# Performance work log

Hardware: AMD Instinct MI355X
Metric: run time of the kernel (lower is better)

Reference implementation:

```python
import jax, jax.numpy as jnp
import numpy as np

BATCH, T, N_STATE, N_CTRL = 16, 512, 64, 32


def setup_inputs() -> dict:
    key = jax.random.key(0)
    ks = jax.random.split(key, 6)
    n, m = N_STATE, N_CTRL
    # SPD per-step cost: Q = M M^T/(n+m) + I  (guarantees Q_uu invertible)
    M = jax.random.normal(ks[0], (BATCH, T, n + m, n + m), jnp.float32)
    Q = jnp.einsum('btij,btkj->btik', M, M) / (n + m) + jnp.eye(n + m, dtype=jnp.float32)
    p = jax.random.normal(ks[1], (BATCH, T, n + m), jnp.float32)
    # near-stable dynamics so the T-step rollout stays bounded
    A = 0.9 * jnp.eye(n, dtype=jnp.float32) + 0.02 * jax.random.normal(ks[2], (BATCH, T, n, n), jnp.float32)
    B = 0.1 * jax.random.normal(ks[3], (BATCH, T, n, m), jnp.float32)
    c1 = 0.1 * jax.random.normal(ks[4], (BATCH, T, n), jnp.float32)
    x_init = jax.random.normal(ks[5], (BATCH, n), jnp.float32)
    return {'Q': Q, 'p': p, 'A': A, 'B': B, 'c1': c1, 'x_init': x_init}


def _lqr(Q, p, A, B, c1, x_init):
    n = A.shape[-1]
    F = jnp.concatenate([A, B], axis=-1)                      # [b,T,n,n+m]
    # time-major for scan
    Qs = jnp.moveaxis(Q, 1, 0)
    ps = jnp.moveaxis(p, 1, 0)
    Fs = jnp.moveaxis(F, 1, 0)
    cs = jnp.moveaxis(c1, 1, 0)
    bsz = x_init.shape[0]
    V0 = jnp.zeros((bsz, n, n), Q.dtype)
    v0 = jnp.zeros((bsz, n), Q.dtype)

    def bstep(carry, inp):
        V, v = carry
        Qt, pt, Ft, ct = inp
        FtV = jnp.einsum('bij,bik->bjk', Ft, V)               # F^T V : [b,n+m,n]
        Qh = Qt + FtV @ Ft                                     # Q_t + F^T V F
        qh = pt + jnp.einsum('bij,bi->bj', Ft,
                             jnp.einsum('bij,bj->bi', V, ct) + v)
        Quu, Qux = Qh[:, n:, n:], Qh[:, n:, :n]
        Qxx, Qxu = Qh[:, :n, :n], Qh[:, :n, n:]
        qx, qu = qh[:, :n], qh[:, n:]
        L = jnp.linalg.cholesky(Quu)
        rhs = jnp.concatenate([Qux, qu[..., None]], axis=-1)   # solve K and k together
        sol = -jax.scipy.linalg.cho_solve((L, True), rhs)
        K, k = sol[..., :n], sol[..., n]
        QuuK = Quu @ K
        Vn = Qxx + Qxu @ K + jnp.einsum('bji,bjk->bik', K, Qux + QuuK)
        Vn = 0.5 * (Vn + jnp.swapaxes(Vn, -1, -2))             # keep symmetric
        vn = qx + jnp.einsum('bij,bj->bi', Qxu, k) \
             + jnp.einsum('bji,bj->bi', K, qu + jnp.einsum('bij,bj->bi', Quu, k))
        return (Vn, vn), (K, k)

    _, (Ks, ks) = jax.lax.scan(bstep, (V0, v0), (Qs, ps, Fs, cs), reverse=True)

    def fstep(x, inp):
        Kt, kt, At, Bt, ct = inp
        u = jnp.einsum('bij,bj->bi', Kt, x) + kt
        xn = jnp.einsum('bij,bj->bi', At, x) + jnp.einsum('bij,bj->bi', Bt, u) + ct
        return xn, (x, u)

    _, (xs, us) = jax.lax.scan(fstep, x_init,
                               (Ks, ks, jnp.moveaxis(A, 1, 0), jnp.moveaxis(B, 1, 0), cs))
    tau = jnp.concatenate([xs, us], axis=-1)                   # [T,b,n+m]
    return jnp.moveaxis(tau, 0, 1)                             # [b,T,n+m]


def reference(Q, p, A, B, c1, x_init):
    return _lqr(Q, p, A, B, c1, x_init)
```

## Files before the change

kernel.cpp:

```cpp
#include <hip/hip_runtime.h>
#include <math.h>

#define TT 512
#define NB 16

#define QH_B   0
#define LI_B   38400
#define T1_B   43008
#define VBH_B  52368
#define VBL_B  61584
#define FTH_B  70800
#define FTL_B  84624
#define WTH_B  98448
#define WTL_B  112272
#define VR_B   98448
#define XUH_B  126096
#define XUL_B  131216
#define KTH_B  136336
#define KTL_B  141456
#define QHF_B  146576
#define VV_B   146960
#define CV_B   147216
#define KV_B   147472
#define SMB    147600

#define AB0 0
#define AB1 6400
#define KF0 12800
#define KF1 14976
#define XB0 17152
#define XB1 17216
#define UBO 17280
#define AXO 17312

#define WSK_STRIDE 2080

typedef __attribute__((ext_vector_type(8))) short s8v;
typedef __attribute__((ext_vector_type(4))) float f4v;

__device__ __forceinline__ float lanebc(float x, int lane) {
    return __int_as_float(__builtin_amdgcn_readlane(__float_as_int(x), lane));
}
__device__ __forceinline__ float dot4(float4 a, float4 b) {
    return a.x * b.x + a.y * b.y + a.z * b.z + a.w * b.w;
}
__device__ __forceinline__ unsigned short f2bf(float x) {
    unsigned int u = __float_as_uint(x);
    u += 0x7FFFu + ((u >> 16) & 1u);
    return (unsigned short)(u >> 16);
}
__device__ __forceinline__ float bf2f(unsigned short h) {
    return __uint_as_float(((unsigned int)h) << 16);
}
__device__ __forceinline__ void tileMN(int T, int& mt, int& nt) {
    mt = (T >= 15) ? 5 : (T >= 10) ? 4 : (T >= 6) ? 3 : (T >= 3) ? 2 : (T >= 1) ? 1 : 0;
    nt = T - mt * (mt + 1) / 2;
}
#define MFMA(a,b,c) __builtin_amdgcn_mfma_f32_16x16x32_bf16((a),(b),(c),0,0,0)

__launch_bounds__(512, 2)
__global__ void lqr_kernel(const float* __restrict__ Q, const float* __restrict__ P,
                           const float* __restrict__ A, const float* __restrict__ B,
                           const float* __restrict__ c1, const float* __restrict__ xinit,
                           float* __restrict__ out, float* __restrict__ ws)
{
    __shared__ __align__(16) unsigned char smb[SMB];
    float*          QHf = (float*)(smb + QH_B);
    float*          LIf = (float*)(smb + LI_B);
    float*          T1f = (float*)(smb + T1_B);
    unsigned short* VBH = (unsigned short*)(smb + VBH_B);
    unsigned short* VBL = (unsigned short*)(smb + VBL_B);
    unsigned short* FTH = (unsigned short*)(smb + FTH_B);
    unsigned short* FTL = (unsigned short*)(smb + FTL_B);
    unsigned short* WTH = (unsigned short*)(smb + WTH_B);
    unsigned short* WTL = (unsigned short*)(smb + WTL_B);
    float*          VRW = (float*)(smb + VR_B);
    unsigned short* XUH = (unsigned short*)(smb + XUH_B);
    unsigned short* XUL = (unsigned short*)(smb + XUL_B);
    unsigned short* KTH = (unsigned short*)(smb + KTH_B);
    unsigned short* KTL = (unsigned short*)(smb + KTL_B);
    float*          QHF = (float*)(smb + QHF_B);
    float*          VVf = (float*)(smb + VV_B);
    float*          CVf = (float*)(smb + CV_B);
    float*          KVf = (float*)(smb + KV_B);

    const int tid = threadIdx.x;
    const int b   = blockIdx.x;
    const int wv  = tid >> 6;
    const int ln  = tid & 63;
    const int l15 = ln & 15;
    const int lq  = ln >> 4;
    float* wsK = ws;

    const int qcnt = (wv < 5) ? 3 : 2;
    const int qr = ln >> 2, qc4 = ln & 3;

    float4 qreg[3];
    {
        const float* Qg = Q + ((size_t)b * TT + (TT - 1)) * 9216;
        for (int tt = 0; tt < qcnt; ++tt) {
            int T = wv + 8 * tt, mt, nt; tileMN(T, mt, nt);
            qreg[tt] = *(const float4*)&Qg[(16 * mt + qr) * 96 + 16 * nt + 4 * qc4];
        }
    }

    if (tid < 384) {
        const size_t bt = (size_t)b * TT + (TT - 1);
        const int kk = tid & 63, cq = tid >> 6;
#pragma unroll
        for (int q = 0; q < 4; ++q) {
            const float* src = (cq < 4) ? (A + (bt * 64 + kk) * 64 + 16 * cq + 4 * q)
                                        : (B + (bt * 64 + kk) * 32 + 16 * (cq - 4) + 4 * q);
            float4 v = *(const float4*)src;
#pragma unroll
            for (int e = 0; e < 4; ++e) {
                int col = 16 * cq + 4 * q + e;
                float x = (e == 0) ? v.x : (e == 1) ? v.y : (e == 2) ? v.z : v.w;
                unsigned short h = f2bf(x);
                FTH[col * 72 + kk] = h;
                FTL[col * 72 + kk] = f2bf(x - bf2f(h));
            }
        }
    } else {
        float* vb = (float*)VBH;
        for (int i = tid - 384; i < 4608; i += 128) vb[i] = 0.0f;
        if (tid >= 448) VVf[tid - 448] = 0.0f;
    }
    __syncthreads();

    for (int t = TT - 1; t >= 0; --t) {
        const size_t bt  = (size_t)b * TT + t;
        const size_t btp = (size_t)b * TT + ((t > 0) ? (t - 1) : 0);

        for (int tt = 0; tt < qcnt; ++tt) {
            int T = wv + 8 * tt, mt, nt; tileMN(T, mt, nt);
            *(float4*)&QHf[(16 * mt + qr) * 100 + 16 * nt + 4 * qc4] = qreg[tt];
        }
        {
            const float* Qg = Q + btp * 9216;
            for (int tt = 0; tt < qcnt; ++tt) {
                int T = wv + 8 * tt, mt, nt; tileMN(T, mt, nt);
                qreg[tt] = *(const float4*)&Qg[(16 * mt + qr) * 96 + 16 * nt + 4 * qc4];
            }
        }
        float4 fp4[4];
        if (wv >= 1 && wv <= 6) {
            const int tau = tid - 64, kk = tau & 63, cq = tau >> 6;
#pragma unroll
            for (int q = 0; q < 4; ++q) {
                const float* src = (cq < 4) ? (A + (btp * 64 + kk) * 64 + 16 * cq + 4 * q)
                                            : (B + (btp * 64 + kk) * 32 + 16 * (cq - 4) + 4 * q);
                fp4[q] = *(const float4*)src;
            }
        }
        if (wv == 7 && ln < 16)
            *(float4*)&CVf[4 * ln] = *(const float4*)&c1[bt * 64 + 4 * ln];
        float pv = 0.0f;
        if (ln < 48 && (ln & 3) == 0) pv = P[bt * 96 + 12 * wv + (ln >> 2)];

        {
#pragma unroll
            for (int tt = 0; tt < 3; ++tt) {
                int T = wv * 3 + tt, mt = T >> 2, nt = T & 3;
                const unsigned short* ah = FTH + (16 * mt + l15) * 72 + 8 * lq;
                const unsigned short* al = FTL + (16 * mt + l15) * 72 + 8 * lq;
                const unsigned short* bh = VBH + (16 * nt + l15) * 72 + 8 * lq;
                const unsigned short* bl = VBL + (16 * nt + l15) * 72 + 8 * lq;
                f4v d = {0.0f, 0.0f, 0.0f, 0.0f};
#pragma unroll
                for (int kc = 0; kc < 2; ++kc) {
                    s8v Ah = *(const s8v*)(ah + 32 * kc);
                    s8v Al = *(const s8v*)(al + 32 * kc);
                    s8v Bh = *(const s8v*)(bh + 32 * kc);
                    s8v Bl = *(const s8v*)(bl + 32 * kc);
                    d = MFMA(Ah, Bh, d);
                    d = MFMA(Ah, Bl, d);
                    d = MFMA(Al, Bh, d);
                }
                int orow = 16 * mt + 4 * lq, ocol = 16 * nt + l15;
#pragma unroll
                for (int rr = 0; rr < 4; ++rr) {
                    float x = d[rr];
                    unsigned short h = f2bf(x);
                    WTH[(orow + rr) * 72 + ocol] = h;
                    WTL[(orow + rr) * 72 + ocol] = f2bf(x - bf2f(h));
                }
            }
            if (ln < 48) {
                int row = 12 * wv + (ln >> 2), kq = ln & 3;
                float acc = 0.0f;
                const unsigned short* fh = FTH + row * 72 + 16 * kq;
                const unsigned short* fl = FTL + row * 72 + 16 * kq;
                const float* vvp = VVf + 16 * kq;
#pragma unroll
                for (int k = 0; k < 16; ++k)
                    acc += (bf2f(fh[k]) + bf2f(fl[k])) * vvp[k];
                acc += __shfl_xor(acc, 1);
                acc += __shfl_xor(acc, 2);
                if ((ln & 3) == 0) QHF[row] = acc + pv;
            }
        }
        __syncthreads();

        {
            for (int tt = 0; tt < qcnt; ++tt) {
                int T = wv + 8 * tt, mt, nt; tileMN(T, mt, nt);
                int orow = 16 * mt + 4 * lq, ocol = 16 * nt + l15;
                const unsigned short* ah = FTH + (16 * mt + l15) * 72 + 8 * lq;
                const unsigned short* al = FTL + (16 * mt + l15) * 72 + 8 * lq;
                const unsigned short* bh = WTH + (16 * nt + l15) * 72 + 8 * lq;
                const unsigned short* bl = WTL + (16 * nt + l15) * 72 + 8 * lq;
                f4v d;
#pragma unroll
                for (int rr = 0; rr < 4; ++rr)
                    d[rr] = QHf[(orow + rr) * 100 + ocol];
#pragma unroll
                for (int kc = 0; kc < 2; ++kc) {
                    s8v Ah = *(const s8v*)(ah + 32 * kc);
                    s8v Al = *(const s8v*)(al + 32 * kc);
                    s8v Bh = *(const s8v*)(bh + 32 * kc);
                    s8v Bl = *(const s8v*)(bl + 32 * kc);
                    d = MFMA(Ah, Bh, d);
                    d = MFMA(Ah, Bl, d);
                    d = MFMA(Al, Bh, d);
                }
#pragma unroll
                for (int rr = 0; rr < 4; ++rr)
                    QHf[(orow + rr) * 100 + ocol] = d[rr];
                if (mt > nt) {
#pragma unroll
                    for (int rr = 0; rr < 4; ++rr)
                        QHf[ocol * 100 + orow + rr] = d[rr];
                }
                if (mt >= 4 && nt < 4) {
#pragma unroll
                    for (int rr = 0; rr < 4; ++rr) {
                        float x = d[rr];
                        unsigned short h = f2bf(x);
                        XUH[ocol * 40 + (orow + rr - 64)] = h;
                        XUL[ocol * 40 + (orow + rr - 64)] = f2bf(x - bf2f(h));
                    }
                }
            }
        }
        __syncthreads();

        if (wv == 0) {
            const int i = ln & 31;
            float a[32], rinv[32];
#pragma unroll
            for (int j4 = 0; j4 < 8; ++j4) {
                float4 v = *(const float4*)&QHf[(64 + i) * 100 + 64 + 4 * j4];
                a[4 * j4] = v.x; a[4 * j4 + 1] = v.y; a[4 * j4 + 2] = v.z; a[4 * j4 + 3] = v.w;
            }
#pragma unroll
            for (int j = 0; j < 32; ++j) {
                float dj = lanebc(a[j], j);
                float rj = rsqrtf(dj);
                rinv[j] = rj;
                a[j] *= rj;
#pragma unroll
                for (int k = j + 1; k < 32; ++k)
                    a[k] -= a[j] * lanebc(a[j], k);
            }
            float y[32];
#pragma unroll
            for (int r = 0; r < 32; ++r) {
                float acc0 = (r == i) ? 1.0f : 0.0f, acc1 = 0.0f;
#pragma unroll
                for (int j = 0; j < r; ++j) {
                    float lrj = lanebc(a[j], r);
                    if (j & 1) acc1 -= lrj * y[j]; else acc0 -= lrj * y[j];
                }
                y[r] = (acc0 + acc1) * rinv[r];
            }
            if (ln < 32) {
#pragma unroll
                for (int r = 0; r < 32; ++r) LIf[r * 36 + ln] = y[r];
            }
        } else if (wv == 7) {
#pragma unroll
            for (int pass = 0; pass < 2; ++pass) {
                int j = pass ? (64 + (ln & 31)) : ln;
                if (pass && ln >= 32) break;
                float acc = QHF[j];
                const unsigned short* wh = WTH + j * 72;
                const unsigned short* wl = WTL + j * 72;
#pragma unroll 4
                for (int i = 0; i < 64; ++i)
                    acc += (bf2f(wh[i]) + bf2f(wl[i])) * CVf[i];
                QHf[j * 100 + 96] = acc;
            }
        } else {
            const int tau = tid - 64, kk = tau & 63, cq = tau >> 6;
#pragma unroll
            for (int q = 0; q < 4; ++q) {
                float4 v = fp4[q];
#pragma unroll
                for (int e = 0; e < 4; ++e) {
                    int col = 16 * cq + 4 * q + e;
                    float x = (e == 0) ? v.x : (e == 1) ? v.y : (e == 2) ? v.z : v.w;
                    unsigned short h = f2bf(x);
                    FTH[col * 72 + kk] = h;
                    FTL[col * 72 + kk] = f2bf(x - bf2f(h));
                }
            }
        }
        __syncthreads();

        {
            const int c = tid & 63, rq = tid >> 6;
            f4v acc = {0.0f, 0.0f, 0.0f, 0.0f};
#pragma unroll
            for (int j4 = 0; j4 < 8; ++j4) {
                float4 qv = *(const float4*)&QHf[c * 100 + 64 + 4 * j4];
#pragma unroll
                for (int rr = 0; rr < 4; ++rr) {
                    float4 li = *(const float4*)&LIf[(4 * rq + rr) * 36 + 4 * j4];
                    acc[rr] += dot4(li, qv);
                }
            }
            *(f4v*)&T1f[c * 36 + 4 * rq] = acc;
            if (tid < 32) {
                float aq = 0.0f;
#pragma unroll 4
                for (int j = 0; j < 32; ++j)
                    aq += LIf[tid * 36 + j] * QHf[(64 + j) * 100 + 96];
                T1f[64 * 36 + tid] = aq;
            }
        }
        __syncthreads();

        {
            const int c = tid & 63, jq = tid >> 6;
            f4v acc = {0.0f, 0.0f, 0.0f, 0.0f};
#pragma unroll
            for (int i4 = 0; i4 < 8; ++i4) {
                float4 tv = *(const float4*)&T1f[c * 36 + 4 * i4];
#pragma unroll
                for (int ii = 0; ii < 4; ++ii) {
                    float4 li = *(const float4*)&LIf[(4 * i4 + ii) * 36 + 4 * jq];
                    float tvi = (ii == 0) ? tv.x : (ii == 1) ? tv.y : (ii == 2) ? tv.z : tv.w;
                    acc[0] += tvi * li.x; acc[1] += tvi * li.y;
                    acc[2] += tvi * li.z; acc[3] += tvi * li.w;
                }
            }
            float* wrow = wsK + bt * WSK_STRIDE;
#pragma unroll
            for (int jj = 0; jj < 4; ++jj) {
                float kval = -acc[jj];
                unsigned short h = f2bf(kval);
                KTH[c * 40 + 4 * jq + jj] = h;
                KTL[c * 40 + 4 * jq + jj] = f2bf(kval - bf2f(h));
                wrow[(4 * jq + jj) * 65 + c] = kval;
            }
            if (tid < 32) {
                float aq = 0.0f;
#pragma unroll 4
                for (int i = 0; i < 32; ++i)
                    aq += LIf[i * 36 + tid] * T1f[64 * 36 + i];
                KVf[tid] = -aq;
                wsK[bt * WSK_STRIDE + tid * 65 + 64] = -aq;
            }
        }
        __syncthreads();

        {
#pragma unroll
            for (int tt = 0; tt < 2; ++tt) {
                int T = 2 * wv + tt, mt = T >> 2, nt = T & 3;
                int orow = 16 * mt + 4 * lq, ocol = 16 * nt + l15;
                f4v d;
#pragma unroll
                for (int rr = 0; rr < 4; ++rr)
                    d[rr] = QHf[(orow + rr) * 100 + ocol];
                s8v Ah = *(const s8v*)(XUH + (16 * mt + l15) * 40 + 8 * lq);
                s8v Al = *(const s8v*)(XUL + (16 * mt + l15) * 40 + 8 * lq);
                s8v Bh = *(const s8v*)(KTH + (16 * nt + l15) * 40 + 8 * lq);
                s8v Bl = *(const s8v*)(KTL + (16 * nt + l15) * 40 + 8 * lq);
                d = MFMA(Ah, Bh, d);
                d = MFMA(Ah, Bl, d);
                d = MFMA(Al, Bh, d);
#pragma unroll
                for (int rr = 0; rr < 4; ++rr)
                    VRW[(orow + rr) * 72 + ocol] = d[rr];
            }
        }
        __syncthreads();

        if (tid < 256) {
            const int rg = tid >> 4, cgv = tid & 15;
            float4 m0[4], m1[4];
#pragma unroll
            for (int rr = 0; rr < 4; ++rr) {
                m0[rr] = *(const float4*)&VRW[(4 * rg + rr) * 72 + 4 * cgv];
                m1[rr] = *(const float4*)&VRW[(4 * cgv + rr) * 72 + 4 * rg];
            }
#pragma unroll
            for (int rr = 0; rr < 4; ++rr) {
                float s[4];
                s[0] = 0.5f * (m0[rr].x + ((float*)&m1[0])[rr]);
                s[1] = 0.5f * (m0[rr].y + ((float*)&m1[1])[rr]);
                s[2] = 0.5f * (m0[rr].z + ((float*)&m1[2])[rr]);
                s[3] = 0.5f * (m0[rr].w + ((float*)&m1[3])[rr]);
                unsigned short h[4], lo[4];
#pragma unroll
                for (int cc = 0; cc < 4; ++cc) {
                    h[cc]  = f2bf(s[cc]);
                    lo[cc] = f2bf(s[cc] - bf2f(h[cc]));
                }
                ushort4 hv = make_ushort4(h[0], h[1], h[2], h[3]);
                ushort4 lv = make_ushort4(lo[0], lo[1], lo[2], lo[3]);
                *(ushort4*)&VBH[(4 * rg + rr) * 72 + 4 * cgv] = hv;
                *(ushort4*)&VBL[(4 * rg + rr) * 72 + 4 * cgv] = lv;
            }
        } else if (tid < 320) {
            const int r = tid & 63;
            float acc = QHf[r * 100 + 96];
#pragma unroll
            for (int j4 = 0; j4 < 8; ++j4) {
                float4 qv = *(const float4*)&QHf[r * 100 + 64 + 4 * j4];
                float4 kv = *(const float4*)&KVf[4 * j4];
                acc += dot4(qv, kv);
            }
            VVf[r] = acc;
        }
        __syncthreads();
    }

    float* sm = (float*)smb;
    {
        const size_t bt0 = (size_t)b * TT;
#pragma unroll
        for (int it = 0; it < 3; ++it) {
            int q = tid + 512 * it, row = q / 24, g = q % 24;
            const float* src = (g < 16) ? (A + (bt0 * 64 + row) * 64 + 4 * g)
                                        : (B + (bt0 * 64 + row) * 32 + 4 * (g - 16));
            *(float4*)&sm[AB0 + row * 100 + 4 * g] = *(const float4*)src;
        }
#pragma unroll
        for (int i = 0; i < 5; ++i) {
            int idx = tid + 512 * i;
            if (idx < 2080) {
                int j = idx / 65, c = idx - 65 * j;
                sm[KF0 + j * 68 + c] = wsK[bt0 * WSK_STRIDE + idx];
            }
        }
        if (tid < 64) sm[XB0 + tid] = xinit[b * 64 + tid];
    }
    __syncthreads();

    for (int t = 0; t < TT; ++t) {
        const size_t bt  = (size_t)b * TT + t;
        const size_t btn = (size_t)b * TT + ((t < TT - 1) ? (t + 1) : t);
        const int cur = t & 1;
        const int abC = cur ? AB1 : AB0, abN = cur ? AB0 : AB1;
        const int kfC = cur ? KF1 : KF0, kfN = cur ? KF0 : KF1;
        const int xbC = cur ? XB1 : XB0, xbN = cur ? XB0 : XB1;

        float4 abpre[6];
        float kpre[9];
        float cpre = 0.0f;
        if (tid >= 256) {
            const int t2 = tid - 256;
#pragma unroll
            for (int it = 0; it < 6; ++it) {
                int q = t2 + 256 * it, row = q / 24, g = q % 24;
                const float* src = (g < 16) ? (A + (btn * 64 + row) * 64 + 4 * g)
                                            : (B + (btn * 64 + row) * 32 + 4 * (g - 16));
                abpre[it] = *(const float4*)src;
            }
#pragma unroll
            for (int i = 0; i < 9; ++i) {
                int idx = t2 + 256 * i;
                kpre[i] = (idx < 2080) ? wsK[btn * WSK_STRIDE + idx] : 0.0f;
            }
            cpre = c1[bt * 64 + ((tid - 256) >> 2)];
        }

        if (tid < 256) {
            const int j = tid >> 3, q = tid & 7;
            float4 k0 = *(const float4*)&sm[kfC + j * 68 + 8 * q];
            float4 k1 = *(const float4*)&sm[kfC + j * 68 + 8 * q + 4];
            float4 x0 = *(const float4*)&sm[xbC + 8 * q];
            float4 x1 = *(const float4*)&sm[xbC + 8 * q + 4];
            float pa = dot4(k0, x0) + dot4(k1, x1);
            pa += __shfl_xor(pa, 1);
            pa += __shfl_xor(pa, 2);
            pa += __shfl_xor(pa, 4);
            if (q == 0) {
                float u = pa + sm[kfC + j * 68 + 64];
                sm[UBO + j] = u;
                out[bt * 96 + 64 + j] = u;
            }
        } else {
            const int r = (tid - 256) >> 2, q = tid & 3;
            float pa = 0.0f;
#pragma unroll
            for (int e4 = 0; e4 < 4; ++e4) {
                float4 av = *(const float4*)&sm[abC + r * 100 + 16 * q + 4 * e4];
                float4 xv = *(const float4*)&sm[xbC + 16 * q + 4 * e4];
                pa += dot4(av, xv);
            }
            pa += __shfl_xor(pa, 1);
            pa += __shfl_xor(pa, 2);
            if (q == 0) sm[AXO + r] = pa + cpre;
            if (q == 1) out[bt * 96 + r] = sm[xbC + r];
        }
        __syncthreads();

        if (tid < 256) {
            const int r = tid >> 2, q = tid & 3;
            float4 b0 = *(const float4*)&sm[abC + r * 100 + 64 + 8 * q];
            float4 b1 = *(const float4*)&sm[abC + r * 100 + 64 + 8 * q + 4];
            float4 u0 = *(const float4*)&sm[UBO + 8 * q];
            float4 u1 = *(const float4*)&sm[UBO + 8 * q + 4];
            float pa = dot4(b0, u0) + dot4(b1, u1);
            pa += __shfl_xor(pa, 1);
            pa += __shfl_xor(pa, 2);
            if (q == 0) sm[xbN + r] = sm[AXO + r] + pa;
        } else {
            const int t2 = tid - 256;
#pragma unroll
            for (int it = 0; it < 6; ++it) {
                int q = t2 + 256 * it, row = q / 24, g = q % 24;
                *(float4*)&sm[abN + row * 100 + 4 * g] = abpre[it];
            }
#pragma unroll
            for (int i = 0; i < 9; ++i) {
                int idx = t2 + 256 * i;
                if (idx < 2080) {
                    int j = idx / 65, c = idx - 65 * j;
                    sm[kfN + j * 68 + c] = kpre[i];
                }
            }
        }
        __syncthreads();
    }
}

extern "C" void kernel_launch(void* const* d_in, const int* in_sizes, int n_in,
                              void* d_out, int out_size, void* d_ws, size_t ws_size,
                              hipStream_t stream) {
    (void)in_sizes; (void)n_in; (void)out_size;
    const float* Q  = (const float*)d_in[0];
    const float* p  = (const float*)d_in[1];
    const float* A  = (const float*)d_in[2];
    const float* B  = (const float*)d_in[3];
    const float* c1 = (const float*)d_in[4];
    const float* xi = (const float*)d_in[5];
    if (ws_size < (size_t)NB * TT * WSK_STRIDE * sizeof(float)) return;
    lqr_kernel<<<NB, 512, 0, stream>>>(Q, p, A, B, c1, xi, (float*)d_out, (float*)d_ws);
}
```

Measured before the change: 9.074 ms.

## Double block size to 1024 threads and redistribute per-step work across 16 waves

Launches the single-block-per-batch LQR kernel with 1024 threads instead of 512 and reassigns every phase of the backward and forward recursions (Q tile loads, F^T V MFMA tiles, vector products, Cholesky-based gain products, V update tiles) across 16 waves. The aim is to shorten the per-timestep serial critical path, since only 16 blocks run and most of the GPU is idle. More threads per block means more barrier cost and less register budget per thread, and many phases now leave some waves idle.

```diff
diff --git a/kernel.cpp b/kernel.cpp
--- a/kernel.cpp
+++ b/kernel.cpp
@@ -58,7 +58,7 @@
 }
 #define MFMA(a,b,c) __builtin_amdgcn_mfma_f32_16x16x32_bf16((a),(b),(c),0,0,0)
 
-__launch_bounds__(512, 2)
+__launch_bounds__(1024, 4)
 __global__ void lqr_kernel(const float* __restrict__ Q, const float* __restrict__ P,
                            const float* __restrict__ A, const float* __restrict__ B,
                            const float* __restrict__ c1, const float* __restrict__ xinit,
@@ -92,29 +92,31 @@
     const int lq  = ln >> 4;
     float* wsK = ws;
 
-    const int qcnt = (wv < 5) ? 3 : 2;
+    const int qcnt = (wv < 5) ? 2 : 1;
     const int qr = ln >> 2, qc4 = ln & 3;
 
-    float4 qreg[3];
+    float4 qreg[2];
     {
         const float* Qg = Q + ((size_t)b * TT + (TT - 1)) * 9216;
-        for (int tt = 0; tt < qcnt; ++tt) {
-            int T = wv + 8 * tt, mt, nt; tileMN(T, mt, nt);
+#pragma unroll
+        for (int tt = 0; tt < 2; ++tt) if (tt < qcnt) {
+            int T = wv + 16 * tt, mt, nt; tileMN(T, mt, nt);
             qreg[tt] = *(const float4*)&Qg[(16 * mt + qr) * 96 + 16 * nt + 4 * qc4];
         }
     }
 
-    if (tid < 384) {
+    if (tid < 768) {
         const size_t bt = (size_t)b * TT + (TT - 1);
         const int kk = tid & 63, cq = tid >> 6;
 #pragma unroll
-        for (int q = 0; q < 4; ++q) {
-            const float* src = (cq < 4) ? (A + (bt * 64 + kk) * 64 + 16 * cq + 4 * q)
-                                        : (B + (bt * 64 + kk) * 32 + 16 * (cq - 4) + 4 * q);
+        for (int q = 0; q < 2; ++q) {
+            int col0 = 8 * cq + 4 * q;
+            const float* src = (col0 < 64) ? (A + (bt * 64 + kk) * 64 + col0)
+                                           : (B + (bt * 64 + kk) * 32 + col0 - 64);
             float4 v = *(const float4*)src;
 #pragma unroll
             for (int e = 0; e < 4; ++e) {
-                int col = 16 * cq + 4 * q + e;
+                int col = col0 + e;
                 float x = (e == 0) ? v.x : (e == 1) ? v.y : (e == 2) ? v.z : v.w;
                 unsigned short h = f2bf(x);
                 FTH[col * 72 + kk] = h;
@@ -123,8 +125,8 @@
         }
     } else {
         float* vb = (float*)VBH;
-        for (int i = tid - 384; i < 4608; i += 128) vb[i] = 0.0f;
-        if (tid >= 448) VVf[tid - 448] = 0.0f;
+        for (int i = tid - 768; i < 4608; i += 256) vb[i] = 0.0f;
+        if (tid >= 768 && tid < 832) VVf[tid - 768] = 0.0f;
     }
     __syncthreads();
 
@@ -132,36 +134,42 @@
         const size_t bt  = (size_t)b * TT + t;
         const size_t btp = (size_t)b * TT + ((t > 0) ? (t - 1) : 0);
 
-        for (int tt = 0; tt < qcnt; ++tt) {
-            int T = wv + 8 * tt, mt, nt; tileMN(T, mt, nt);
+#pragma unroll
+        for (int tt = 0; tt < 2; ++tt) if (tt < qcnt) {
+            int T = wv + 16 * tt, mt, nt; tileMN(T, mt, nt);
             *(float4*)&QHf[(16 * mt + qr) * 100 + 16 * nt + 4 * qc4] = qreg[tt];
         }
         {
             const float* Qg = Q + btp * 9216;
-            for (int tt = 0; tt < qcnt; ++tt) {
-                int T = wv + 8 * tt, mt, nt; tileMN(T, mt, nt);
+#pragma unroll
+            for (int tt = 0; tt < 2; ++tt) if (tt < qcnt) {
+                int T = wv + 16 * tt, mt, nt; tileMN(T, mt, nt);
                 qreg[tt] = *(const float4*)&Qg[(16 * mt + qr) * 96 + 16 * nt + 4 * qc4];
             }
         }
-        float4 fp4[4];
-        if (wv >= 1 && wv <= 6) {
+        float4 fp4[2];
+        if (wv >= 1 && wv <= 12) {
             const int tau = tid - 64, kk = tau & 63, cq = tau >> 6;
 #pragma unroll
-            for (int q = 0; q < 4; ++q) {
-                const float* src = (cq < 4) ? (A + (btp * 64 + kk) * 64 + 16 * cq + 4 * q)
-                                            : (B + (btp * 64 + kk) * 32 + 16 * (cq - 4) + 4 * q);
+            for (int q = 0; q < 2; ++q) {
+                int col0 = 8 * cq + 4 * q;
+                const float* src = (col0 < 64) ? (A + (btp * 64 + kk) * 64 + col0)
+                                               : (B + (btp * 64 + kk) * 32 + col0 - 64);
                 fp4[q] = *(const float4*)src;
             }
         }
-        if (wv == 7 && ln < 16)
+        if (wv == 13 && ln < 16)
             *(float4*)&CVf[4 * ln] = *(const float4*)&c1[bt * 64 + 4 * ln];
         float pv = 0.0f;
-        if (ln < 48 && (ln & 3) == 0) pv = P[bt * 96 + 12 * wv + (ln >> 2)];
+        if (wv < 12 && (ln & 7) == 0) pv = P[bt * 96 + 8 * wv + (ln >> 3)];
 
         {
-#pragma unroll
-            for (int tt = 0; tt < 3; ++tt) {
-                int T = wv * 3 + tt, mt = T >> 2, nt = T & 3;
+            int t1l[2]; int nT1;
+            if (wv < 8) { t1l[0] = 2 * wv; t1l[1] = 2 * wv + 1; nT1 = 2; }
+            else        { t1l[0] = 8 + wv; t1l[1] = 0;          nT1 = 1; }
+#pragma unroll
+            for (int tt = 0; tt < 2; ++tt) if (tt < nT1) {
+                int T = t1l[tt], mt = T >> 2, nt = T & 3;
                 const unsigned short* ah = FTH + (16 * mt + l15) * 72 + 8 * lq;
                 const unsigned short* al = FTL + (16 * mt + l15) * 72 + 8 * lq;
                 const unsigned short* bh = VBH + (16 * nt + l15) * 72 + 8 * lq;
@@ -186,25 +194,27 @@
                     WTL[(orow + rr) * 72 + ocol] = f2bf(x - bf2f(h));
                 }
             }
-            if (ln < 48) {
-                int row = 12 * wv + (ln >> 2), kq = ln & 3;
+            if (wv < 12) {
+                int row = 8 * wv + (ln >> 3), kq = ln & 7;
                 float acc = 0.0f;
-                const unsigned short* fh = FTH + row * 72 + 16 * kq;
-                const unsigned short* fl = FTL + row * 72 + 16 * kq;
-                const float* vvp = VVf + 16 * kq;
-#pragma unroll
-                for (int k = 0; k < 16; ++k)
+                const unsigned short* fh = FTH + row * 72 + 8 * kq;
+                const unsigned short* fl = FTL + row * 72 + 8 * kq;
+                const float* vvp = VVf + 8 * kq;
+#pragma unroll
+                for (int k = 0; k < 8; ++k)
                     acc += (bf2f(fh[k]) + bf2f(fl[k])) * vvp[k];
                 acc += __shfl_xor(acc, 1);
                 acc += __shfl_xor(acc, 2);
-                if ((ln & 3) == 0) QHF[row] = acc + pv;
+                acc += __shfl_xor(acc, 4);
+                if ((ln & 7) == 0) QHF[row] = acc + pv;
             }
         }
         __syncthreads();
 
         {
-            for (int tt = 0; tt < qcnt; ++tt) {
-                int T = wv + 8 * tt, mt, nt; tileMN(T, mt, nt);
+#pragma unroll
+            for (int tt = 0; tt < 2; ++tt) if (tt < qcnt) {
+                int T = wv + 16 * tt, mt, nt; tileMN(T, mt, nt);
                 int orow = 16 * mt + 4 * lq, ocol = 16 * nt + l15;
                 const unsigned short* ah = FTH + (16 * mt + l15) * 72 + 8 * lq;
                 const unsigned short* al = FTL + (16 * mt + l15) * 72 + 8 * lq;
@@ -278,11 +288,9 @@
 #pragma unroll
                 for (int r = 0; r < 32; ++r) LIf[r * 36 + ln] = y[r];
             }
-        } else if (wv == 7) {
-#pragma unroll
-            for (int pass = 0; pass < 2; ++pass) {
-                int j = pass ? (64 + (ln & 31)) : ln;
-                if (pass && ln >= 32) break;
+        } else if (wv >= 14) {
+            int j = (wv == 14) ? ln : (64 + (ln & 31));
+            if (wv == 14 || ln < 32) {
                 float acc = QHF[j];
                 const unsigned short* wh = WTH + j * 72;
                 const unsigned short* wl = WTL + j * 72;
@@ -291,14 +299,15 @@
                     acc += (bf2f(wh[i]) + bf2f(wl[i])) * CVf[i];
                 QHf[j * 100 + 96] = acc;
             }
-        } else {
+        } else if (wv <= 12) {
             const int tau = tid - 64, kk = tau & 63, cq = tau >> 6;
 #pragma unroll
-            for (int q = 0; q < 4; ++q) {
+            for (int q = 0; q < 2; ++q) {
                 float4 v = fp4[q];
+                int col0 = 8 * cq + 4 * q;
 #pragma unroll
                 for (int e = 0; e < 4; ++e) {
-                    int col = 16 * cq + 4 * q + e;
+                    int col = col0 + e;
                     float x = (e == 0) ? v.x : (e == 1) ? v.y : (e == 2) ? v.z : v.w;
                     unsigned short h = f2bf(x);
                     FTH[col * 72 + kk] = h;
@@ -309,18 +318,17 @@
         __syncthreads();
 
         {
-            const int c = tid & 63, rq = tid >> 6;
-            f4v acc = {0.0f, 0.0f, 0.0f, 0.0f};
+            const int c = tid & 63, g = tid >> 6;
+            float a0 = 0.0f, a1 = 0.0f;
 #pragma unroll
             for (int j4 = 0; j4 < 8; ++j4) {
                 float4 qv = *(const float4*)&QHf[c * 100 + 64 + 4 * j4];
-#pragma unroll
-                for (int rr = 0; rr < 4; ++rr) {
-                    float4 li = *(const float4*)&LIf[(4 * rq + rr) * 36 + 4 * j4];
-                    acc[rr] += dot4(li, qv);
-                }
-            }
-            *(f4v*)&T1f[c * 36 + 4 * rq] = acc;
+                float4 l0 = *(const float4*)&LIf[(2 * g) * 36 + 4 * j4];
+                float4 l1 = *(const float4*)&LIf[(2 * g + 1) * 36 + 4 * j4];
+                a0 += dot4(l0, qv);
+                a1 += dot4(l1, qv);
+            }
+            *(float2*)&T1f[c * 36 + 2 * g] = make_float2(a0, a1);
             if (tid < 32) {
                 float aq = 0.0f;
 #pragma unroll 4
@@ -332,28 +340,26 @@
         __syncthreads();
 
         {
-            const int c = tid & 63, jq = tid >> 6;
-            f4v acc = {0.0f, 0.0f, 0.0f, 0.0f};
+            const int c = tid & 63, g = tid >> 6;
+            float a0 = 0.0f, a1 = 0.0f;
 #pragma unroll
             for (int i4 = 0; i4 < 8; ++i4) {
                 float4 tv = *(const float4*)&T1f[c * 36 + 4 * i4];
 #pragma unroll
                 for (int ii = 0; ii < 4; ++ii) {
-                    float4 li = *(const float4*)&LIf[(4 * i4 + ii) * 36 + 4 * jq];
+                    float2 li = *(const float2*)&LIf[(4 * i4 + ii) * 36 + 2 * g];
                     float tvi = (ii == 0) ? tv.x : (ii == 1) ? tv.y : (ii == 2) ? tv.z : tv.w;
-                    acc[0] += tvi * li.x; acc[1] += tvi * li.y;
-                    acc[2] += tvi * li.z; acc[3] += tvi * li.w;
-                }
-            }
+                    a0 += tvi * li.x;
+                    a1 += tvi * li.y;
+                }
+            }
+            float k0 = -a0, k1 = -a1;
+            unsigned short h0 = f2bf(k0), h1 = f2bf(k1);
+            *(ushort2*)&KTH[c * 40 + 2 * g] = make_ushort2(h0, h1);
+            *(ushort2*)&KTL[c * 40 + 2 * g] = make_ushort2(f2bf(k0 - bf2f(h0)), f2bf(k1 - bf2f(h1)));
             float* wrow = wsK + bt * WSK_STRIDE;
-#pragma unroll
-            for (int jj = 0; jj < 4; ++jj) {
-                float kval = -acc[jj];
-                unsigned short h = f2bf(kval);
-                KTH[c * 40 + 4 * jq + jj] = h;
-                KTL[c * 40 + 4 * jq + jj] = f2bf(kval - bf2f(h));
-                wrow[(4 * jq + jj) * 65 + c] = kval;
-            }
+            wrow[(2 * g) * 65 + c]     = k0;
+            wrow[(2 * g + 1) * 65 + c] = k1;
             if (tid < 32) {
                 float aq = 0.0f;
 #pragma unroll 4
@@ -366,25 +372,22 @@
         __syncthreads();
 
         {
-#pragma unroll
-            for (int tt = 0; tt < 2; ++tt) {
-                int T = 2 * wv + tt, mt = T >> 2, nt = T & 3;
-                int orow = 16 * mt + 4 * lq, ocol = 16 * nt + l15;
-                f4v d;
-#pragma unroll
-                for (int rr = 0; rr < 4; ++rr)
-                    d[rr] = QHf[(orow + rr) * 100 + ocol];
-                s8v Ah = *(const s8v*)(XUH + (16 * mt + l15) * 40 + 8 * lq);
-                s8v Al = *(const s8v*)(XUL + (16 * mt + l15) * 40 + 8 * lq);
-                s8v Bh = *(const s8v*)(KTH + (16 * nt + l15) * 40 + 8 * lq);
-                s8v Bl = *(const s8v*)(KTL + (16 * nt + l15) * 40 + 8 * lq);
-                d = MFMA(Ah, Bh, d);
-                d = MFMA(Ah, Bl, d);
-                d = MFMA(Al, Bh, d);
-#pragma unroll
-                for (int rr = 0; rr < 4; ++rr)
-                    VRW[(orow + rr) * 72 + ocol] = d[rr];
-            }
+            int mt = wv >> 2, nt = wv & 3;
+            int orow = 16 * mt + 4 * lq, ocol = 16 * nt + l15;
+            f4v d;
+#pragma unroll
+            for (int rr = 0; rr < 4; ++rr)
+                d[rr] = QHf[(orow + rr) * 100 + ocol];
+            s8v Ah = *(const s8v*)(XUH + (16 * mt + l15) * 40 + 8 * lq);
+            s8v Al = *(const s8v*)(XUL + (16 * mt + l15) * 40 + 8 * lq);
+            s8v Bh = *(const s8v*)(KTH + (16 * nt + l15) * 40 + 8 * lq);
+            s8v Bl = *(const s8v*)(KTL + (16 * nt + l15) * 40 + 8 * lq);
+            d = MFMA(Ah, Bh, d);
+            d = MFMA(Ah, Bl, d);
+            d = MFMA(Al, Bh, d);
+#pragma unroll
+            for (int rr = 0; rr < 4; ++rr)
+                VRW[(orow + rr) * 72 + ocol] = d[rr];
         }
         __syncthreads();
 
@@ -432,15 +435,18 @@
     {
         const size_t bt0 = (size_t)b * TT;
 #pragma unroll
-        for (int it = 0; it < 3; ++it) {
-            int q = tid + 512 * it, row = q / 24, g = q % 24;
-            const float* src = (g < 16) ? (A + (bt0 * 64 + row) * 64 + 4 * g)
-                                        : (B + (bt0 * 64 + row) * 32 + 4 * (g - 16));
-            *(float4*)&sm[AB0 + row * 100 + 4 * g] = *(const float4*)src;
-        }
-#pragma unroll
-        for (int i = 0; i < 5; ++i) {
-            int idx = tid + 512 * i;
+        for (int it = 0; it < 2; ++it) {
+            int q = tid + 1024 * it;
+            if (q < 1536) {
+                int row = q / 24, g = q % 24;
+                const float* src = (g < 16) ? (A + (bt0 * 64 + row) * 64 + 4 * g)
+                                            : (B + (bt0 * 64 + row) * 32 + 4 * (g - 16));
+                *(float4*)&sm[AB0 + row * 100 + 4 * g] = *(const float4*)src;
+            }
+        }
+#pragma unroll
+        for (int i = 0; i < 3; ++i) {
+            int idx = tid + 1024 * i;
             if (idx < 2080) {
                 int j = idx / 65, c = idx - 65 * j;
                 sm[KF0 + j * 68 + c] = wsK[bt0 * WSK_STRIDE + idx];
@@ -461,8 +467,8 @@
         float4 abpre[6];
         float kpre[9];
         float cpre = 0.0f;
-        if (tid >= 256) {
-            const int t2 = tid - 256;
+        if (tid >= 512 && tid < 768) {
+            const int t2 = tid - 512;
 #pragma unroll
             for (int it = 0; it < 6; ++it) {
                 int q = t2 + 256 * it, row = q / 24, g = q % 24;
@@ -475,8 +481,9 @@
                 int idx = t2 + 256 * i;
                 kpre[i] = (idx < 2080) ? wsK[btn * WSK_STRIDE + idx] : 0.0f;
             }
+        }
+        if (tid >= 256 && tid < 512)
             cpre = c1[bt * 64 + ((tid - 256) >> 2)];
-        }
 
         if (tid < 256) {
             const int j = tid >> 3, q = tid & 7;
@@ -493,7 +500,7 @@
                 sm[UBO + j] = u;
                 out[bt * 96 + 64 + j] = u;
             }
-        } else {
+        } else if (tid < 512) {
             const int r = (tid - 256) >> 2, q = tid & 3;
             float pa = 0.0f;
 #pragma unroll
@@ -519,8 +526,8 @@
             pa += __shfl_xor(pa, 1);
             pa += __shfl_xor(pa, 2);
             if (q == 0) sm[xbN + r] = sm[AXO + r] + pa;
-        } else {
-            const int t2 = tid - 256;
+        } else if (tid >= 512 && tid < 768) {
+            const int t2 = tid - 512;
 #pragma unroll
             for (int it = 0; it < 6; ++it) {
                 int q = t2 + 256 * it, row = q / 24, g = q % 24;
@@ -550,5 +557,5 @@
     const float* c1 = (const float*)d_in[4];
     const float* xi = (const float*)d_in[5];
     if (ws_size < (size_t)NB * TT * WSK_STRIDE * sizeof(float)) return;
-    lqr_kernel<<<NB, 512, 0, stream>>>(Q, p, A, B, c1, xi, (float*)d_out, (float*)d_ws);
-}
+    lqr_kernel<<<NB, 1024, 0, stream>>>(Q, p, A, B, c1, xi, (float*)d_out, (float*)d_ws);
+}
```

After: 11.63 ms. +28.1%, slower.

## Restructure backward step schedule to cut barriers and rebalance wave work

Applied to the files above, without the earlier changes.

Qh tile products are redistributed so waves overlap them with the Cholesky wave, F-conversion is moved into the K-solve stage, and the two-stage K computation is merged into one stage using a transposed inverse-L copy. The separate symmetrization pass for V is dropped: V is written straight to bf16 hi/lo from the MFMA output, and the value-vector update uses a shuffle reduction. This removes two block barriers per time step and reshapes the shared-memory layout. Skipping explicit symmetrization means V relies on the algebraic symmetry of the result, which may slightly change numerics.

```diff
diff --git a/kernel.cpp b/kernel.cpp
--- a/kernel.cpp
+++ b/kernel.cpp
@@ -6,23 +6,23 @@
 
 #define QH_B   0
 #define LI_B   38400
-#define T1_B   43008
-#define VBH_B  52368
-#define VBL_B  61584
-#define FTH_B  70800
-#define FTL_B  84624
-#define WTH_B  98448
-#define WTL_B  112272
-#define VR_B   98448
-#define XUH_B  126096
-#define XUL_B  131216
-#define KTH_B  136336
-#define KTL_B  141456
-#define QHF_B  146576
-#define VV_B   146960
-#define CV_B   147216
-#define KV_B   147472
-#define SMB    147600
+#define LIT_B  43008
+#define KV_B   47616
+#define VBH_B  47744
+#define VBL_B  56960
+#define FTH_B  66176
+#define FTL_B  80000
+#define WTH_B  93824
+#define WTL_B  107648
+#define T1S_B  93824
+#define XUH_B  121472
+#define XUL_B  126592
+#define KTH_B  131712
+#define KTL_B  136832
+#define QHF_B  141952
+#define VV_B   142336
+#define CV_B   142592
+#define SMB    142848
 
 #define AB0 0
 #define AB1 6400
@@ -67,14 +67,14 @@
     __shared__ __align__(16) unsigned char smb[SMB];
     float*          QHf = (float*)(smb + QH_B);
     float*          LIf = (float*)(smb + LI_B);
-    float*          T1f = (float*)(smb + T1_B);
+    float*          LIT = (float*)(smb + LIT_B);
+    float*          T1S = (float*)(smb + T1S_B);
     unsigned short* VBH = (unsigned short*)(smb + VBH_B);
     unsigned short* VBL = (unsigned short*)(smb + VBL_B);
     unsigned short* FTH = (unsigned short*)(smb + FTH_B);
     unsigned short* FTL = (unsigned short*)(smb + FTL_B);
     unsigned short* WTH = (unsigned short*)(smb + WTH_B);
     unsigned short* WTL = (unsigned short*)(smb + WTL_B);
-    float*          VRW = (float*)(smb + VR_B);
     unsigned short* XUH = (unsigned short*)(smb + XUH_B);
     unsigned short* XUL = (unsigned short*)(smb + XUL_B);
     unsigned short* KTH = (unsigned short*)(smb + KTH_B);
@@ -98,7 +98,8 @@
     float4 qreg[3];
     {
         const float* Qg = Q + ((size_t)b * TT + (TT - 1)) * 9216;
-        for (int tt = 0; tt < qcnt; ++tt) {
+#pragma unroll
+        for (int tt = 0; tt < 3; ++tt) if (tt < qcnt) {
             int T = wv + 8 * tt, mt, nt; tileMN(T, mt, nt);
             qreg[tt] = *(const float4*)&Qg[(16 * mt + qr) * 96 + 16 * nt + 4 * qc4];
         }
@@ -132,20 +133,22 @@
         const size_t bt  = (size_t)b * TT + t;
         const size_t btp = (size_t)b * TT + ((t > 0) ? (t - 1) : 0);
 
-        for (int tt = 0; tt < qcnt; ++tt) {
+#pragma unroll
+        for (int tt = 0; tt < 3; ++tt) if (tt < qcnt) {
             int T = wv + 8 * tt, mt, nt; tileMN(T, mt, nt);
             *(float4*)&QHf[(16 * mt + qr) * 100 + 16 * nt + 4 * qc4] = qreg[tt];
         }
         {
             const float* Qg = Q + btp * 9216;
-            for (int tt = 0; tt < qcnt; ++tt) {
+#pragma unroll
+            for (int tt = 0; tt < 3; ++tt) if (tt < qcnt) {
                 int T = wv + 8 * tt, mt, nt; tileMN(T, mt, nt);
                 qreg[tt] = *(const float4*)&Qg[(16 * mt + qr) * 96 + 16 * nt + 4 * qc4];
             }
         }
         float4 fp4[4];
-        if (wv >= 1 && wv <= 6) {
-            const int tau = tid - 64, kk = tau & 63, cq = tau >> 6;
+        if (tid >= 128) {
+            const int tau = tid - 128, kk = tau & 63, cq = tau >> 6;
 #pragma unroll
             for (int q = 0; q < 4; ++q) {
                 const float* src = (cq < 4) ? (A + (btp * 64 + kk) * 64 + 16 * cq + 4 * q)
@@ -157,6 +160,46 @@
             *(float4*)&CVf[4 * ln] = *(const float4*)&c1[bt * 64 + 4 * ln];
         float pv = 0.0f;
         if (ln < 48 && (ln & 3) == 0) pv = P[bt * 96 + 12 * wv + (ln >> 2)];
+
+        auto qhTile = [&](int T) {
+            int mt, nt; tileMN(T, mt, nt);
+            int orow = 16 * mt + 4 * lq, ocol = 16 * nt + l15;
+            const unsigned short* ah = FTH + (16 * mt + l15) * 72 + 8 * lq;
+            const unsigned short* al = FTL + (16 * mt + l15) * 72 + 8 * lq;
+            const unsigned short* bh = WTH + (16 * nt + l15) * 72 + 8 * lq;
+            const unsigned short* bl = WTL + (16 * nt + l15) * 72 + 8 * lq;
+            f4v d;
+#pragma unroll
+            for (int rr = 0; rr < 4; ++rr)
+                d[rr] = QHf[(orow + rr) * 100 + ocol];
+#pragma unroll
+            for (int kc = 0; kc < 2; ++kc) {
+                s8v Ah = *(const s8v*)(ah + 32 * kc);
+                s8v Al = *(const s8v*)(al + 32 * kc);
+                s8v Bh = *(const s8v*)(bh + 32 * kc);
+                s8v Bl = *(const s8v*)(bl + 32 * kc);
+                d = MFMA(Ah, Bh, d);
+                d = MFMA(Ah, Bl, d);
+                d = MFMA(Al, Bh, d);
+            }
+#pragma unroll
+            for (int rr = 0; rr < 4; ++rr)
+                QHf[(orow + rr) * 100 + ocol] = d[rr];
+            if (mt > nt) {
+#pragma unroll
+                for (int rr = 0; rr < 4; ++rr)
+                    QHf[ocol * 100 + orow + rr] = d[rr];
+            }
+            if (mt >= 4 && nt < 4) {
+#pragma unroll
+                for (int rr = 0; rr < 4; ++rr) {
+                    float x = d[rr];
+                    unsigned short h = f2bf(x);
+                    XUH[ocol * 40 + (orow + rr - 64)] = h;
+                    XUL[ocol * 40 + (orow + rr - 64)] = f2bf(x - bf2f(h));
+                }
+            }
+        };
 
         {
 #pragma unroll
@@ -203,51 +246,16 @@
         __syncthreads();
 
         {
-            for (int tt = 0; tt < qcnt; ++tt) {
-                int T = wv + 8 * tt, mt, nt; tileMN(T, mt, nt);
-                int orow = 16 * mt + 4 * lq, ocol = 16 * nt + l15;
-                const unsigned short* ah = FTH + (16 * mt + l15) * 72 + 8 * lq;
-                const unsigned short* al = FTL + (16 * mt + l15) * 72 + 8 * lq;
-                const unsigned short* bh = WTH + (16 * nt + l15) * 72 + 8 * lq;
-                const unsigned short* bl = WTL + (16 * nt + l15) * 72 + 8 * lq;
-                f4v d;
-#pragma unroll
-                for (int rr = 0; rr < 4; ++rr)
-                    d[rr] = QHf[(orow + rr) * 100 + ocol];
-#pragma unroll
-                for (int kc = 0; kc < 2; ++kc) {
-                    s8v Ah = *(const s8v*)(ah + 32 * kc);
-                    s8v Al = *(const s8v*)(al + 32 * kc);
-                    s8v Bh = *(const s8v*)(bh + 32 * kc);
-                    s8v Bl = *(const s8v*)(bl + 32 * kc);
-                    d = MFMA(Ah, Bh, d);
-                    d = MFMA(Ah, Bl, d);
-                    d = MFMA(Al, Bh, d);
-                }
-#pragma unroll
-                for (int rr = 0; rr < 4; ++rr)
-                    QHf[(orow + rr) * 100 + ocol] = d[rr];
-                if (mt > nt) {
-#pragma unroll
-                    for (int rr = 0; rr < 4; ++rr)
-                        QHf[ocol * 100 + orow + rr] = d[rr];
-                }
-                if (mt >= 4 && nt < 4) {
-#pragma unroll
-                    for (int rr = 0; rr < 4; ++rr) {
-                        float x = d[rr];
-                        unsigned short h = f2bf(x);
-                        XUH[ocol * 40 + (orow + rr - 64)] = h;
-                        XUL[ocol * 40 + (orow + rr - 64)] = f2bf(x - bf2f(h));
-                    }
-                }
-            }
+            int T = (wv == 0) ? 14 : (wv == 1) ? 19 : (wv == 2) ? 20 :
+                    (wv == 3) ? 0  : (wv == 4) ? 1  : (wv == 5) ? 2  :
+                    (wv == 6) ? 3  : 4;
+            qhTile(T);
         }
         __syncthreads();
 
         if (wv == 0) {
             const int i = ln & 31;
-            float a[32], rinv[32];
+            float a[32];
 #pragma unroll
             for (int j4 = 0; j4 < 8; ++j4) {
                 float4 v = *(const float4*)&QHf[(64 + i) * 100 + 64 + 4 * j4];
@@ -257,7 +265,6 @@
             for (int j = 0; j < 32; ++j) {
                 float dj = lanebc(a[j], j);
                 float rj = rsqrtf(dj);
-                rinv[j] = rj;
                 a[j] *= rj;
 #pragma unroll
                 for (int k = j + 1; k < 32; ++k)
@@ -272,95 +279,121 @@
                     float lrj = lanebc(a[j], r);
                     if (j & 1) acc1 -= lrj * y[j]; else acc0 -= lrj * y[j];
                 }
-                y[r] = (acc0 + acc1) * rinv[r];
+                y[r] = (acc0 + acc1) * __builtin_amdgcn_rcpf(lanebc(a[r], r));
             }
             if (ln < 32) {
 #pragma unroll
                 for (int r = 0; r < 32; ++r) LIf[r * 36 + ln] = y[r];
-            }
-        } else if (wv == 7) {
-#pragma unroll
-            for (int pass = 0; pass < 2; ++pass) {
-                int j = pass ? (64 + (ln & 31)) : ln;
-                if (pass && ln >= 32) break;
-                float acc = QHF[j];
-                const unsigned short* wh = WTH + j * 72;
-                const unsigned short* wl = WTL + j * 72;
+#pragma unroll
+                for (int r4 = 0; r4 < 8; ++r4)
+                    *(float4*)&LIT[ln * 36 + 4 * r4] =
+                        make_float4(y[4 * r4], y[4 * r4 + 1], y[4 * r4 + 2], y[4 * r4 + 3]);
+            }
+        } else {
+            const int Ta = (wv == 1) ? 5 : (wv == 2) ? 7 : (wv == 3) ? 9 :
+                           (wv == 4) ? 11 : (wv == 5) ? 13 : (wv == 6) ? 16 : 18;
+            qhTile(Ta);
+            if (wv <= 6) {
+                const int Tb = (wv == 1) ? 6 : (wv == 2) ? 8 : (wv == 3) ? 10 :
+                               (wv == 4) ? 12 : (wv == 5) ? 15 : 17;
+                qhTile(Tb);
+            } else {
+#pragma unroll
+                for (int pass = 0; pass < 2; ++pass) {
+                    int j = pass ? (64 + (ln & 31)) : ln;
+                    if (pass && ln >= 32) break;
+                    float acc = QHF[j];
+                    const unsigned short* wh = WTH + j * 72;
+                    const unsigned short* wl = WTL + j * 72;
 #pragma unroll 4
-                for (int i = 0; i < 64; ++i)
-                    acc += (bf2f(wh[i]) + bf2f(wl[i])) * CVf[i];
-                QHf[j * 100 + 96] = acc;
-            }
-        } else {
-            const int tau = tid - 64, kk = tau & 63, cq = tau >> 6;
-#pragma unroll
-            for (int q = 0; q < 4; ++q) {
-                float4 v = fp4[q];
-#pragma unroll
-                for (int e = 0; e < 4; ++e) {
-                    int col = 16 * cq + 4 * q + e;
-                    float x = (e == 0) ? v.x : (e == 1) ? v.y : (e == 2) ? v.z : v.w;
-                    unsigned short h = f2bf(x);
-                    FTH[col * 72 + kk] = h;
-                    FTL[col * 72 + kk] = f2bf(x - bf2f(h));
+                    for (int i = 0; i < 64; ++i)
+                        acc += (bf2f(wh[i]) + bf2f(wl[i])) * CVf[i];
+                    QHf[j * 100 + 96] = acc;
                 }
             }
         }
         __syncthreads();
 
         {
-            const int c = tid & 63, rq = tid >> 6;
-            f4v acc = {0.0f, 0.0f, 0.0f, 0.0f};
-#pragma unroll
-            for (int j4 = 0; j4 < 8; ++j4) {
-                float4 qv = *(const float4*)&QHf[c * 100 + 64 + 4 * j4];
-#pragma unroll
-                for (int rr = 0; rr < 4; ++rr) {
-                    float4 li = *(const float4*)&LIf[(4 * rq + rr) * 36 + 4 * j4];
-                    acc[rr] += dot4(li, qv);
-                }
-            }
-            *(f4v*)&T1f[c * 36 + 4 * rq] = acc;
-            if (tid < 32) {
-                float aq = 0.0f;
-#pragma unroll 4
-                for (int j = 0; j < 32; ++j)
-                    aq += LIf[tid * 36 + j] * QHf[(64 + j) * 100 + 96];
-                T1f[64 * 36 + tid] = aq;
-            }
-        }
-        __syncthreads();
-
-        {
-            const int c = tid & 63, jq = tid >> 6;
-            f4v acc = {0.0f, 0.0f, 0.0f, 0.0f};
-#pragma unroll
-            for (int i4 = 0; i4 < 8; ++i4) {
-                float4 tv = *(const float4*)&T1f[c * 36 + 4 * i4];
-#pragma unroll
-                for (int ii = 0; ii < 4; ++ii) {
-                    float4 li = *(const float4*)&LIf[(4 * i4 + ii) * 36 + 4 * jq];
-                    float tvi = (ii == 0) ? tv.x : (ii == 1) ? tv.y : (ii == 2) ? tv.z : tv.w;
-                    acc[0] += tvi * li.x; acc[1] += tvi * li.y;
-                    acc[2] += tvi * li.z; acc[3] += tvi * li.w;
-                }
-            }
+            const int g = tid >> 3, q = tid & 7;
+            float4 qc[8];
+#pragma unroll
+            for (int j4 = 0; j4 < 8; ++j4)
+                qc[j4] = *(const float4*)&QHf[g * 100 + 64 + 4 * j4];
+            float t1v[4];
+#pragma unroll
+            for (int s = 0; s < 4; ++s) {
+                float acc = 0.0f;
+#pragma unroll
+                for (int j4 = 0; j4 < 8; ++j4)
+                    acc += dot4(*(const float4*)&LIf[(4 * q + s) * 36 + 4 * j4], qc[j4]);
+                t1v[s] = acc;
+            }
+            *(float4*)&T1S[g * 36 + 4 * q] = make_float4(t1v[0], t1v[1], t1v[2], t1v[3]);
+            float4 ts[8];
+#pragma unroll
+            for (int i4 = 0; i4 < 8; ++i4)
+                ts[i4] = *(const float4*)&T1S[g * 36 + 4 * i4];
             float* wrow = wsK + bt * WSK_STRIDE;
 #pragma unroll
-            for (int jj = 0; jj < 4; ++jj) {
-                float kval = -acc[jj];
-                unsigned short h = f2bf(kval);
-                KTH[c * 40 + 4 * jq + jj] = h;
-                KTL[c * 40 + 4 * jq + jj] = f2bf(kval - bf2f(h));
-                wrow[(4 * jq + jj) * 65 + c] = kval;
-            }
-            if (tid < 32) {
-                float aq = 0.0f;
-#pragma unroll 4
-                for (int i = 0; i < 32; ++i)
-                    aq += LIf[i * 36 + tid] * T1f[64 * 36 + i];
-                KVf[tid] = -aq;
-                wsK[bt * WSK_STRIDE + tid * 65 + 64] = -aq;
+            for (int s = 0; s < 4; ++s) {
+                int r = 4 * q + s;
+                float acc = 0.0f;
+#pragma unroll
+                for (int i4 = 0; i4 < 8; ++i4)
+                    acc += dot4(*(const float4*)&LIT[r * 36 + 4 * i4], ts[i4]);
+                float kv = -acc;
+                unsigned short h = f2bf(kv);
+                KTH[g * 40 + r] = h;
+                KTL[g * 40 + r] = f2bf(kv - bf2f(h));
+                wrow[r * 65 + g] = kv;
+            }
+            if (g == 0) {
+                float t1q[4];
+#pragma unroll
+                for (int s = 0; s < 4; ++s) {
+                    float acc = 0.0f;
+#pragma unroll
+                    for (int j4 = 0; j4 < 8; ++j4) {
+                        float4 li = *(const float4*)&LIf[(4 * q + s) * 36 + 4 * j4];
+                        float4 qv = make_float4(QHf[(64 + 4 * j4) * 100 + 96],
+                                                QHf[(65 + 4 * j4) * 100 + 96],
+                                                QHf[(66 + 4 * j4) * 100 + 96],
+                                                QHf[(67 + 4 * j4) * 100 + 96]);
+                        acc += dot4(li, qv);
+                    }
+                    t1q[s] = acc;
+                }
+                *(float4*)&T1S[64 * 36 + 4 * q] = make_float4(t1q[0], t1q[1], t1q[2], t1q[3]);
+                float4 tq[8];
+#pragma unroll
+                for (int i4 = 0; i4 < 8; ++i4)
+                    tq[i4] = *(const float4*)&T1S[64 * 36 + 4 * i4];
+#pragma unroll
+                for (int s = 0; s < 4; ++s) {
+                    int r = 4 * q + s;
+                    float acc = 0.0f;
+#pragma unroll
+                    for (int i4 = 0; i4 < 8; ++i4)
+                        acc += dot4(*(const float4*)&LIT[r * 36 + 4 * i4], tq[i4]);
+                    KVf[r] = -acc;
+                    wrow[r * 65 + 64] = -acc;
+                }
+            }
+            if (tid >= 128) {
+                const int tau = tid - 128, kk = tau & 63, cq = tau >> 6;
+#pragma unroll
+                for (int q2 = 0; q2 < 4; ++q2) {
+                    float4 v = fp4[q2];
+#pragma unroll
+                    for (int e = 0; e < 4; ++e) {
+                        int col = 16 * cq + 4 * q2 + e;
+                        float x = (e == 0) ? v.x : (e == 1) ? v.y : (e == 2) ? v.z : v.w;
+                        unsigned short h = f2bf(x);
+                        FTH[col * 72 + kk] = h;
+                        FTL[col * 72 + kk] = f2bf(x - bf2f(h));
+                    }
+                }
             }
         }
         __syncthreads();
@@ -382,48 +415,26 @@
                 d = MFMA(Ah, Bl, d);
                 d = MFMA(Al, Bh, d);
 #pragma unroll
-                for (int rr = 0; rr < 4; ++rr)
-                    VRW[(orow + rr) * 72 + ocol] = d[rr];
-            }
-        }
-        __syncthreads();
-
-        if (tid < 256) {
-            const int rg = tid >> 4, cgv = tid & 15;
-            float4 m0[4], m1[4];
-#pragma unroll
-            for (int rr = 0; rr < 4; ++rr) {
-                m0[rr] = *(const float4*)&VRW[(4 * rg + rr) * 72 + 4 * cgv];
-                m1[rr] = *(const float4*)&VRW[(4 * cgv + rr) * 72 + 4 * rg];
-            }
-#pragma unroll
-            for (int rr = 0; rr < 4; ++rr) {
-                float s[4];
-                s[0] = 0.5f * (m0[rr].x + ((float*)&m1[0])[rr]);
-                s[1] = 0.5f * (m0[rr].y + ((float*)&m1[1])[rr]);
-                s[2] = 0.5f * (m0[rr].z + ((float*)&m1[2])[rr]);
-                s[3] = 0.5f * (m0[rr].w + ((float*)&m1[3])[rr]);
-                unsigned short h[4], lo[4];
-#pragma unroll
-                for (int cc = 0; cc < 4; ++cc) {
-                    h[cc]  = f2bf(s[cc]);
-                    lo[cc] = f2bf(s[cc] - bf2f(h[cc]));
-                }
-                ushort4 hv = make_ushort4(h[0], h[1], h[2], h[3]);
-                ushort4 lv = make_ushort4(lo[0], lo[1], lo[2], lo[3]);
-                *(ushort4*)&VBH[(4 * rg + rr) * 72 + 4 * cgv] = hv;
-                *(ushort4*)&VBL[(4 * rg + rr) * 72 + 4 * cgv] = lv;
-            }
-        } else if (tid < 320) {
-            const int r = tid & 63;
-            float acc = QHf[r * 100 + 96];
-#pragma unroll
-            for (int j4 = 0; j4 < 8; ++j4) {
-                float4 qv = *(const float4*)&QHf[r * 100 + 64 + 4 * j4];
-                float4 kv = *(const float4*)&KVf[4 * j4];
-                acc += dot4(qv, kv);
-            }
-            VVf[r] = acc;
+                for (int rr = 0; rr < 4; ++rr) {
+                    float x = d[rr];
+                    unsigned short h = f2bf(x);
+                    VBH[(orow + rr) * 72 + ocol] = h;
+                    VBL[(orow + rr) * 72 + ocol] = f2bf(x - bf2f(h));
+                }
+            }
+            {
+                int r = 8 * wv + (ln >> 3), kq = ln & 7;
+                float acc = 0.0f;
+#pragma unroll
+                for (int e = 0; e < 4; ++e) {
+                    int j = 4 * kq + e;
+                    acc += QHf[r * 100 + 64 + j] * KVf[j];
+                }
+                acc += __shfl_xor(acc, 1);
+                acc += __shfl_xor(acc, 2);
+                acc += __shfl_xor(acc, 4);
+                if (kq == 0) VVf[r] = acc + QHf[r * 100 + 96];
+            }
         }
         __syncthreads();
     }
```

After: 11.28 ms. +24.3%, slower.
